# Performance work log

Measured on AMD Instinct MI355X. Metric: run time of the kernel, lower is better.

The kernel has to match this reference:

```python
import jax, jax.numpy as jnp
import numpy as np

KERNELS = [(1, 2), (2, 1), (1, 3), (3, 1), (1, 4), (4, 1), (2, 2)]
IN_C, OUT_C = 16, 64
FC_IN, FC_H1, FC_H2, NUM_ACTIONS = 3648, 512, 128, 4


def setup_inputs() -> dict:
    key = jax.random.key(0)
    ks = jax.random.split(key, 32)
    B = 32768
    inp = {"x": jax.random.normal(ks[0], (B, IN_C, 4, 4), dtype=jnp.float32)}
    # conv params, OIHW layout, scaled like torch default init (~1/sqrt(fan_in))
    for i, (kh, kw) in enumerate(KERNELS):
        fan_in = IN_C * kh * kw
        s = 1.0 / np.sqrt(fan_in)
        inp[f"w{i}"] = jax.random.uniform(ks[1 + 2 * i], (OUT_C, IN_C, kh, kw), jnp.float32, -s, s)
        inp[f"b{i}"] = jax.random.uniform(ks[2 + 2 * i], (OUT_C,), jnp.float32, -s, s)
    dims = [(FC_IN, FC_H1), (FC_H1, FC_H2), (FC_H2, NUM_ACTIONS)]
    for j, (din, dout) in enumerate(dims):
        s = 1.0 / np.sqrt(din)
        inp[f"fw{j}"] = jax.random.uniform(ks[15 + 2 * j], (dout, din), jnp.float32, -s, s)
        inp[f"fb{j}"] = jax.random.uniform(ks[16 + 2 * j], (dout,), jnp.float32, -s, s)
    return inp


def _conv_relu_flat(x, w, b):
    # x: [B,16,4,4] NCHW, w: [64,16,kh,kw] OIHW -> flatten to [B, 64*oh*ow]
    y = jax.lax.conv_general_dilated(
        x, w, window_strides=(1, 1), padding="VALID",
        dimension_numbers=("NCHW", "OIHW", "NCHW"))
    y = jax.nn.relu(y + b[None, :, None, None])
    return y.reshape(y.shape[0], -1)


def reference(x, w0, b0, w1, b1, w2, b2, w3, b3, w4, b4, w5, b5, w6, b6,
              fw0, fb0, fw1, fb1, fw2, fb2):
    x = x.reshape(-1, 16, 4, 4).astype(jnp.float32)
    ws = [w0, w1, w2, w3, w4, w5, w6]
    bs = [b0, b1, b2, b3, b4, b5, b6]
    combined = jnp.concatenate(
        [_conv_relu_flat(x, w, b) for w, b in zip(ws, bs)], axis=1)  # [B, 3648]
    h = jax.nn.relu(combined @ fw0.T + fb0)
    h = jax.nn.relu(h @ fw1.T + fb1)
    return h @ fw2.T + fb2
```

## Files before the change

kernel.cpp:

```cpp
#include <hip/hip_runtime.h>
#include <hip/hip_bf16.h>
#include <stdint.h>

typedef __attribute__((ext_vector_type(8))) short s8v;
typedef __attribute__((ext_vector_type(4))) float f32x4;

__device__ __forceinline__ unsigned short f2bf(float f) {
  unsigned u = __builtin_bit_cast(unsigned, f);
  u += 0x7fffu + ((u >> 16) & 1u);
  return (unsigned short)(u >> 16);
}

__device__ __forceinline__ void gl16(const void* g, void* l) {
  __builtin_amdgcn_global_load_lds(
      (const __attribute__((address_space(1))) unsigned int*)g,
      (__attribute__((address_space(3))) unsigned int*)l,
      16, 0, 0);
}


__global__ void cast_bf16_k(const float* __restrict__ s, unsigned short* __restrict__ d, int n4) {
  int i = blockIdx.x * blockDim.x + threadIdx.x;
  if (i < n4) {
    float4 v = reinterpret_cast<const float4*>(s)[i];
    ushort4 o;
    o.x = f2bf(v.x); o.y = f2bf(v.y); o.z = f2bf(v.z); o.w = f2bf(v.w);
    reinterpret_cast<ushort4*>(d)[i] = o;
  }
}

__global__ void prep_conv(
    const float* w0, const float* w1, const float* w2, const float* w3,
    const float* w4, const float* w5, const float* w6,
    const float* b0, const float* b1, const float* b2, const float* b3,
    const float* b4, const float* b5, const float* b6,
    unsigned short* __restrict__ Mt, float* __restrict__ cbias)
{
  int n = blockIdx.x * blockDim.x + threadIdx.x;
  if (n >= 3712) return;
  unsigned short* row = Mt + n * 256;
  for (int i = 0; i < 256; ++i) row[i] = 0;
  if (n >= 3648) { cbias[n] = 0.f; return; }
  const int khs[7] = {1,2,1,3,1,4,2};
  const int kws[7] = {2,1,3,1,4,1,2};
  const int cs[8]  = {0,768,1536,2048,2560,2816,3072,3648};
  const float* ws[7] = {w0,w1,w2,w3,w4,w5,w6};
  const float* bs[7] = {b0,b1,b2,b3,b4,b5,b6};
  int k = 6;
  while (n < cs[k]) --k;
  const int kh = khs[k], kw = kws[k];
  const int ow = 5 - kw, np = (5 - kh) * ow;
  const int r = n - cs[k];
  const int och = r / np, p = r % np;
  const int oi = p / ow, oj = p % ow;
  const float* w = ws[k];
  cbias[n] = bs[k][och];
  for (int c = 0; c < 16; ++c)
    for (int dh = 0; dh < kh; ++dh)
      for (int dw = 0; dw < kw; ++dw)
        row[c * 16 + (oi + dh) * 4 + (oj + dw)] =
            f2bf(w[((och * 16 + c) * kh + dh) * kw + dw]);
}

__global__ void prep_fw0(const float* __restrict__ fw0, unsigned short* __restrict__ outp) {
  int idx = blockIdx.x * 256 + threadIdx.x;
  int nrow = idx / 3712;
  int k = idx - nrow * 3712;
  outp[idx] = (k < 3648) ? f2bf(fw0[nrow * 3648 + k]) : (unsigned short)0;
}

__global__ __launch_bounds__(512, 2) void fused_conv_fc1(
    const unsigned short* __restrict__ xb,
    const unsigned short* __restrict__ Mt,
    const float* __restrict__ cbias,
    const unsigned short* __restrict__ fw0b,
    const float* __restrict__ fb0,
    unsigned short* __restrict__ h1)
{
  __shared__ unsigned short xs[128 * 256];
  __shared__ unsigned short ms[128 * 128];
  __shared__ unsigned short ps[128 * 128];
  const int tid = threadIdx.x;
  const int lane = tid & 63;
  const int w = tid >> 6;
  const int wm = w >> 2;
  const int wn = w & 3;
  const int g8 = lane >> 4;
  const int l15 = lane & 15;
  const int m0 = blockIdx.x * 128;

  {
    char* dst = (char*)xs + (w * 8) * 1024 + lane * 16;
#pragma unroll
    for (int i = 0; i < 8; ++i) {
      int c = (w * 8 + i) * 64 + lane;
      int row = c >> 5, col16 = c & 31;
      int cs = col16 ^ (row & 7);
      gl16(xb + (size_t)(m0 + row) * 256 + cs * 8, dst + i * 1024);
    }
  }

  f32x4 acc[4][8] = {};

#pragma unroll 1
  for (int j = 0; j < 29; ++j) {
    f32x4 accp[4][2] = {};
    const int ar = wm * 64 + l15;
    const int br = wn * 32 + l15;
#pragma unroll 1
    for (int h = 0; h < 2; ++h) {
      __syncthreads();
      {
        char* dst = (char*)ms + (w * 4) * 1024 + lane * 16;
#pragma unroll
        for (int i = 0; i < 4; ++i) {
          int c = (w * 4 + i) * 64 + lane;
          int row = c >> 4, col16 = c & 15;
          int cs = col16 ^ (row & 7);
          gl16(Mt + (size_t)(j * 128 + row) * 256 + h * 128 + cs * 8, dst + i * 1024);
        }
      }
      __syncthreads();
#pragma unroll
      for (int kk = 0; kk < 4; ++kk) {
        const int cx = h * 16 + kk * 4 + g8;
        const int cm = kk * 4 + g8;
        s8v xa[4], mb[2];
#pragma unroll
        for (int mi = 0; mi < 4; ++mi) {
          int r = ar + mi * 16;
          xa[mi] = *(const s8v*)((const char*)xs + r * 512 + ((cx ^ (r & 7)) << 4));
        }
#pragma unroll
        for (int ni = 0; ni < 2; ++ni) {
          int r = br + ni * 16;
          mb[ni] = *(const s8v*)((const char*)ms + r * 256 + ((cm ^ (r & 7)) << 4));
        }
#pragma unroll
        for (int mi = 0; mi < 4; ++mi)
#pragma unroll
          for (int ni = 0; ni < 2; ++ni)
            accp[mi][ni] = __builtin_amdgcn_mfma_f32_16x16x32_bf16(
                xa[mi], mb[ni], accp[mi][ni], 0, 0, 0);
      }
    }
#pragma unroll
    for (int ni = 0; ni < 2; ++ni) {
      const int pc = wn * 32 + ni * 16 + l15;
      const float bv = cbias[j * 128 + pc];
#pragma unroll
      for (int mi = 0; mi < 4; ++mi) {
#pragma unroll
        for (int r = 0; r < 4; ++r) {
          const int pr = wm * 64 + mi * 16 + g8 * 4 + r;
          float v = accp[mi][ni][r] + bv;
          v = v > 0.f ? v : 0.f;
          *(unsigned short*)((char*)ps + pr * 256 +
                             (((pc >> 3) ^ (pr & 7)) << 4) + (pc & 7) * 2) = f2bf(v);
        }
      }
    }
    __syncthreads();

    const int kbase = j * 128;
#pragma unroll
    for (int kk = 0; kk < 4; ++kk) {
      const int c16 = kk * 4 + g8;
      s8v pa[4], fwb[8];
#pragma unroll
      for (int mi = 0; mi < 4; ++mi) {
        int r = wm * 64 + mi * 16 + l15;
        pa[mi] = *(const s8v*)((const char*)ps + r * 256 + ((c16 ^ (r & 7)) << 4));
      }
      const int kf = kbase + kk * 32 + g8 * 8;
#pragma unroll
      for (int ni = 0; ni < 8; ++ni) {
        int bn = wn * 128 + ni * 16 + l15;
        fwb[ni] = *(const s8v*)(fw0b + (size_t)bn * 3712 + kf);
      }
#pragma unroll
      for (int mi = 0; mi < 4; ++mi)
#pragma unroll
        for (int ni = 0; ni < 8; ++ni)
          acc[mi][ni] = __builtin_amdgcn_mfma_f32_16x16x32_bf16(
              pa[mi], fwb[ni], acc[mi][ni], 0, 0, 0);
    }
  }

#pragma unroll
  for (int ni = 0; ni < 8; ++ni) {
    const int col = wn * 128 + ni * 16 + l15;
    const float bv = fb0[col];
#pragma unroll
    for (int mi = 0; mi < 4; ++mi) {
      const int row = m0 + wm * 64 + mi * 16 + g8 * 4;
#pragma unroll
      for (int r = 0; r < 4; ++r) {
        float v = acc[mi][ni][r] + bv;
        v = v > 0.f ? v : 0.f;
        h1[(size_t)(row + r) * 512 + col] = f2bf(v);
      }
    }
  }
}

__global__ __launch_bounds__(256) void fc23(
    const unsigned short* __restrict__ h1,
    const unsigned short* __restrict__ fw1b,
    const float* __restrict__ fb1,
    const float* __restrict__ fw2,
    const float* __restrict__ fb2,
    float* __restrict__ out)
{
  __shared__ unsigned short As[64 * 64];
  __shared__ unsigned short Bs[128 * 64];
  __shared__ float h2[64][129];
  const int tid = threadIdx.x;
  const int lane = tid & 63;
  const int wave = tid >> 6;
  const int wm = wave >> 1, wn = wave & 1;
  const int m0 = blockIdx.x * 64;

  f32x4 acc[2][4] = {};

  const unsigned short* Ag = h1 + (size_t)(m0 + (lane >> 3)) * 512 + (lane & 7) * 8;
  const unsigned short* Bg = fw1b + (size_t)(lane >> 3) * 512 + (lane & 7) * 8;
  char* Asb = (char*)As + wave * 2048 + lane * 16;
  char* Bsb = (char*)Bs + wave * 4096 + lane * 16;

  for (int k0 = 0; k0 < 512; k0 += 64) {
#pragma unroll
    for (int i = 0; i < 2; ++i)
      gl16(Ag + (size_t)((wave * 2 + i) * 8) * 512 + k0, Asb + i * 1024);
#pragma unroll
    for (int i = 0; i < 4; ++i)
      gl16(Bg + (size_t)((wave * 4 + i) * 8) * 512 + k0, Bsb + i * 1024);
    __syncthreads();
    const int arow = wm * 32 + (lane & 15);
    const int brow = wn * 64 + (lane & 15);
    const int kc = (lane >> 4) * 8;
    s8v af[2][2], bfv[4][2];
#pragma unroll
    for (int mi = 0; mi < 2; ++mi)
#pragma unroll
      for (int kk = 0; kk < 2; ++kk)
        af[mi][kk] = *(const s8v*)(As + (arow + mi * 16) * 64 + kk * 32 + kc);
#pragma unroll
    for (int ni = 0; ni < 4; ++ni)
#pragma unroll
      for (int kk = 0; kk < 2; ++kk)
        bfv[ni][kk] = *(const s8v*)(Bs + (brow + ni * 16) * 64 + kk * 32 + kc);
#pragma unroll
    for (int kk = 0; kk < 2; ++kk)
#pragma unroll
      for (int mi = 0; mi < 2; ++mi)
#pragma unroll
        for (int ni = 0; ni < 4; ++ni)
          acc[mi][ni] = __builtin_amdgcn_mfma_f32_16x16x32_bf16(
              af[mi][kk], bfv[ni][kk], acc[mi][ni], 0, 0, 0);
    __syncthreads();
  }

#pragma unroll
  for (int ni = 0; ni < 4; ++ni) {
    const int col = wn * 64 + ni * 16 + (lane & 15);
    const float bv = fb1[col];
#pragma unroll
    for (int mi = 0; mi < 2; ++mi) {
      const int rl = wm * 32 + mi * 16 + (lane >> 4) * 4;
#pragma unroll
      for (int r = 0; r < 4; ++r) {
        float v = acc[mi][ni][r] + bv;
        h2[rl + r][col] = v > 0.f ? v : 0.f;
      }
    }
  }
  __syncthreads();

  const int r = tid >> 2, j = tid & 3;
  const float* w = fw2 + j * 128;
  float dot = fb2[j];
#pragma unroll 8
  for (int c = 0; c < 128; ++c) dot += h2[r][c] * w[c];
  out[(size_t)(m0 + r) * 4 + j] = dot;
}


extern "C" void kernel_launch(void* const* d_in, const int* in_sizes, int n_in,
                              void* d_out, int out_size, void* d_ws, size_t ws_size,
                              hipStream_t stream) {
  const float* x = (const float*)d_in[0];
  const float* w[7];
  const float* b[7];
  for (int i = 0; i < 7; ++i) {
    w[i] = (const float*)d_in[1 + 2 * i];
    b[i] = (const float*)d_in[2 + 2 * i];
  }
  const float* fw0 = (const float*)d_in[15];
  const float* fb0 = (const float*)d_in[16];
  const float* fw1 = (const float*)d_in[17];
  const float* fb1 = (const float*)d_in[18];
  const float* fw2 = (const float*)d_in[19];
  const float* fb2 = (const float*)d_in[20];

  char* ws = (char*)d_ws;
  size_t off = 0;
  auto alloc = [&](size_t bytes) {
    void* p = ws + off;
    off += (bytes + 255) & ~(size_t)255;
    return p;
  };
  unsigned short* Mt   = (unsigned short*)alloc((size_t)3712 * 256 * 2);
  float*          cb   = (float*)alloc((size_t)3712 * 4);
  unsigned short* fw0b = (unsigned short*)alloc((size_t)512 * 3712 * 2);
  unsigned short* fw1b = (unsigned short*)alloc((size_t)128 * 512 * 2);
  unsigned short* xb   = (unsigned short*)alloc((size_t)32768 * 256 * 2);
  unsigned short* h1   = (unsigned short*)alloc((size_t)32768 * 512 * 2);
  if (ws_size < off) return;

  cast_bf16_k<<<8192, 256, 0, stream>>>(x, xb, 2097152);
  cast_bf16_k<<<64, 256, 0, stream>>>(fw1, fw1b, 16384);
  prep_conv<<<15, 256, 0, stream>>>(w[0], w[1], w[2], w[3], w[4], w[5], w[6],
                                    b[0], b[1], b[2], b[3], b[4], b[5], b[6], Mt, cb);
  prep_fw0<<<7424, 256, 0, stream>>>(fw0, fw0b);

  fused_conv_fc1<<<256, 512, 0, stream>>>(xb, Mt, cb, fw0b, fb0, h1);
  fc23<<<512, 256, 0, stream>>>(h1, fw1b, fb1, fw2, fb2, (float*)d_out);
}
```

Before: 584.4 us.

## Halve fused conv-FC1 row tile and double-buffer conv matrix staging

```diff
diff --git a/kernel.cpp b/kernel.cpp
--- a/kernel.cpp
+++ b/kernel.cpp
@@ -77,9 +77,10 @@
     const float* __restrict__ fb0,
     unsigned short* __restrict__ h1)
 {
-  __shared__ unsigned short xs[128 * 256];
-  __shared__ unsigned short ms[128 * 128];
-  __shared__ unsigned short ps[128 * 128];
+  __shared__ unsigned short xs[64 * 256];
+  __shared__ unsigned short ms0[128 * 128];
+  __shared__ unsigned short ms1[128 * 128];
+  __shared__ unsigned short ps[64 * 128];
   const int tid = threadIdx.x;
   const int lane = tid & 63;
   const int w = tid >> 6;
@@ -87,72 +88,98 @@
   const int wn = w & 3;
   const int g8 = lane >> 4;
   const int l15 = lane & 15;
-  const int m0 = blockIdx.x * 128;
+  const int m0 = blockIdx.x * 64;
+
+  auto stage_ms = [&](unsigned short* ms, int jj, int h) {
+    char* dst = (char*)ms + (w * 4) * 1024 + lane * 16;
+#pragma unroll
+    for (int i = 0; i < 4; ++i) {
+      int c = (w * 4 + i) * 64 + lane;
+      int row = c >> 4, col16 = c & 15;
+      gl16(Mt + (size_t)(jj * 128 + row) * 256 + h * 128 + (col16 ^ (row & 7)) * 8,
+           dst + i * 1024);
+    }
+  };
 
   {
-    char* dst = (char*)xs + (w * 8) * 1024 + lane * 16;
-#pragma unroll
-    for (int i = 0; i < 8; ++i) {
-      int c = (w * 8 + i) * 64 + lane;
+    char* dst = (char*)xs + (w * 4) * 1024 + lane * 16;
+#pragma unroll
+    for (int i = 0; i < 4; ++i) {
+      int c = (w * 4 + i) * 64 + lane;
       int row = c >> 5, col16 = c & 31;
-      int cs = col16 ^ (row & 7);
-      gl16(xb + (size_t)(m0 + row) * 256 + cs * 8, dst + i * 1024);
-    }
-  }
-
-  f32x4 acc[4][8] = {};
+      gl16(xb + (size_t)(m0 + row) * 256 + (col16 ^ (row & 7)) * 8, dst + i * 1024);
+    }
+  }
+  stage_ms(ms0, 0, 0);
+  stage_ms(ms1, 0, 1);
+  __syncthreads();
+
+  f32x4 acc[2][8] = {};
+  const int ar = wm * 32 + l15;
 
 #pragma unroll 1
   for (int j = 0; j < 29; ++j) {
-    f32x4 accp[4][2] = {};
-    const int ar = wm * 64 + l15;
-    const int br = wn * 32 + l15;
-#pragma unroll 1
-    for (int h = 0; h < 2; ++h) {
-      __syncthreads();
-      {
-        char* dst = (char*)ms + (w * 4) * 1024 + lane * 16;
-#pragma unroll
-        for (int i = 0; i < 4; ++i) {
-          int c = (w * 4 + i) * 64 + lane;
-          int row = c >> 4, col16 = c & 15;
-          int cs = col16 ^ (row & 7);
-          gl16(Mt + (size_t)(j * 128 + row) * 256 + h * 128 + cs * 8, dst + i * 1024);
-        }
-      }
-      __syncthreads();
-#pragma unroll
-      for (int kk = 0; kk < 4; ++kk) {
-        const int cx = h * 16 + kk * 4 + g8;
-        const int cm = kk * 4 + g8;
-        s8v xa[4], mb[2];
-#pragma unroll
-        for (int mi = 0; mi < 4; ++mi) {
-          int r = ar + mi * 16;
-          xa[mi] = *(const s8v*)((const char*)xs + r * 512 + ((cx ^ (r & 7)) << 4));
-        }
-#pragma unroll
-        for (int ni = 0; ni < 2; ++ni) {
-          int r = br + ni * 16;
-          mb[ni] = *(const s8v*)((const char*)ms + r * 256 + ((cm ^ (r & 7)) << 4));
-        }
-#pragma unroll
-        for (int mi = 0; mi < 4; ++mi)
-#pragma unroll
-          for (int ni = 0; ni < 2; ++ni)
-            accp[mi][ni] = __builtin_amdgcn_mfma_f32_16x16x32_bf16(
-                xa[mi], mb[ni], accp[mi][ni], 0, 0, 0);
-      }
-    }
+    const int jn = (j < 28) ? j + 1 : 0;
+    f32x4 accp[2][2] = {};
+
+#pragma unroll
+    for (int kk = 0; kk < 4; ++kk) {
+      const int cx = kk * 4 + g8;
+      s8v xa[2], mb[2];
+#pragma unroll
+      for (int mi = 0; mi < 2; ++mi) {
+        int r = ar + mi * 16;
+        xa[mi] = *(const s8v*)((const char*)xs + r * 512 + ((cx ^ (r & 7)) << 4));
+      }
+#pragma unroll
+      for (int ni = 0; ni < 2; ++ni) {
+        int r = wn * 32 + ni * 16 + l15;
+        mb[ni] = *(const s8v*)((const char*)ms0 + r * 256 + ((cx ^ (r & 7)) << 4));
+      }
+#pragma unroll
+      for (int mi = 0; mi < 2; ++mi)
+#pragma unroll
+        for (int ni = 0; ni < 2; ++ni)
+          accp[mi][ni] = __builtin_amdgcn_mfma_f32_16x16x32_bf16(
+              xa[mi], mb[ni], accp[mi][ni], 0, 0, 0);
+    }
+    __syncthreads();
+
+    stage_ms(ms0, jn, 0);
+
+#pragma unroll
+    for (int kk = 0; kk < 4; ++kk) {
+      const int cm = kk * 4 + g8;
+      const int cx = 16 + cm;
+      s8v xa[2], mb[2];
+#pragma unroll
+      for (int mi = 0; mi < 2; ++mi) {
+        int r = ar + mi * 16;
+        xa[mi] = *(const s8v*)((const char*)xs + r * 512 + ((cx ^ (r & 7)) << 4));
+      }
+#pragma unroll
+      for (int ni = 0; ni < 2; ++ni) {
+        int r = wn * 32 + ni * 16 + l15;
+        mb[ni] = *(const s8v*)((const char*)ms1 + r * 256 + ((cm ^ (r & 7)) << 4));
+      }
+#pragma unroll
+      for (int mi = 0; mi < 2; ++mi)
+#pragma unroll
+        for (int ni = 0; ni < 2; ++ni)
+          accp[mi][ni] = __builtin_amdgcn_mfma_f32_16x16x32_bf16(
+              xa[mi], mb[ni], accp[mi][ni], 0, 0, 0);
+    }
+    __syncthreads();
+
 #pragma unroll
     for (int ni = 0; ni < 2; ++ni) {
       const int pc = wn * 32 + ni * 16 + l15;
       const float bv = cbias[j * 128 + pc];
 #pragma unroll
-      for (int mi = 0; mi < 4; ++mi) {
+      for (int mi = 0; mi < 2; ++mi) {
 #pragma unroll
         for (int r = 0; r < 4; ++r) {
-          const int pr = wm * 64 + mi * 16 + g8 * 4 + r;
+          const int pr = wm * 32 + mi * 16 + g8 * 4 + r;
           float v = accp[mi][ni][r] + bv;
           v = v > 0.f ? v : 0.f;
           *(unsigned short*)((char*)ps + pr * 256 +
@@ -162,24 +189,25 @@
     }
     __syncthreads();
 
-    const int kbase = j * 128;
+    stage_ms(ms1, jn, 1);
+
 #pragma unroll
     for (int kk = 0; kk < 4; ++kk) {
       const int c16 = kk * 4 + g8;
-      s8v pa[4], fwb[8];
-#pragma unroll
-      for (int mi = 0; mi < 4; ++mi) {
-        int r = wm * 64 + mi * 16 + l15;
+      s8v pa[2], fwb[8];
+#pragma unroll
+      for (int mi = 0; mi < 2; ++mi) {
+        int r = wm * 32 + mi * 16 + l15;
         pa[mi] = *(const s8v*)((const char*)ps + r * 256 + ((c16 ^ (r & 7)) << 4));
       }
-      const int kf = kbase + kk * 32 + g8 * 8;
+      const int kf = j * 128 + kk * 32 + g8 * 8;
 #pragma unroll
       for (int ni = 0; ni < 8; ++ni) {
         int bn = wn * 128 + ni * 16 + l15;
         fwb[ni] = *(const s8v*)(fw0b + (size_t)bn * 3712 + kf);
       }
 #pragma unroll
-      for (int mi = 0; mi < 4; ++mi)
+      for (int mi = 0; mi < 2; ++mi)
 #pragma unroll
         for (int ni = 0; ni < 8; ++ni)
           acc[mi][ni] = __builtin_amdgcn_mfma_f32_16x16x32_bf16(
@@ -192,8 +220,8 @@
     const int col = wn * 128 + ni * 16 + l15;
     const float bv = fb0[col];
 #pragma unroll
-    for (int mi = 0; mi < 4; ++mi) {
-      const int row = m0 + wm * 64 + mi * 16 + g8 * 4;
+    for (int mi = 0; mi < 2; ++mi) {
+      const int row = m0 + wm * 32 + mi * 16 + g8 * 4;
 #pragma unroll
       for (int r = 0; r < 4; ++r) {
         float v = acc[mi][ni][r] + bv;
@@ -324,6 +352,6 @@
                                     b[0], b[1], b[2], b[3], b[4], b[5], b[6], Mt, cb);
   prep_fw0<<<7424, 256, 0, stream>>>(fw0, fw0b);
 
-  fused_conv_fc1<<<256, 512, 0, stream>>>(xb, Mt, cb, fw0b, fb0, h1);
+  fused_conv_fc1<<<512, 512, 0, stream>>>(xb, Mt, cb, fw0b, fb0, h1);
   fc23<<<512, 256, 0, stream>>>(h1, fw1b, fb1, fw2, fb2, (float*)d_out);
 }
```

New measurement: 704.5 us. +20.6%, slower.

## Prepack weights into MFMA fragment order and pipeline conv with FC1 tiles

Applied to the files above, without the earlier changes.

```diff
diff --git a/kernel.cpp b/kernel.cpp
--- a/kernel.cpp
+++ b/kernel.cpp
@@ -29,130 +29,124 @@
   }
 }
 
-__global__ void prep_conv(
+__global__ void prep_convF(
     const float* w0, const float* w1, const float* w2, const float* w3,
     const float* w4, const float* w5, const float* w6,
     const float* b0, const float* b1, const float* b2, const float* b3,
     const float* b4, const float* b5, const float* b6,
-    unsigned short* __restrict__ Mt, float* __restrict__ cbias)
+    unsigned short* __restrict__ MtF, float* __restrict__ cbias)
 {
   int n = blockIdx.x * blockDim.x + threadIdx.x;
   if (n >= 3712) return;
-  unsigned short* row = Mt + n * 256;
-  for (int i = 0; i < 256; ++i) row[i] = 0;
+  const int j = n >> 7, nn = n & 127, tile = nn >> 4, ln = nn & 15;
+  auto put = [&](int k, unsigned short v) {
+    int kk = k >> 5, gk = (k >> 3) & 3, e = k & 7;
+    MtF[(size_t)((((j * 8 + kk) * 8 + tile) * 64 + ln * 4 + gk) * 8 + e)] = v;
+  };
+  for (int k = 0; k < 256; ++k) put(k, 0);
   if (n >= 3648) { cbias[n] = 0.f; return; }
   const int khs[7] = {1,2,1,3,1,4,2};
   const int kws[7] = {2,1,3,1,4,1,2};
   const int cs[8]  = {0,768,1536,2048,2560,2816,3072,3648};
   const float* ws[7] = {w0,w1,w2,w3,w4,w5,w6};
   const float* bs[7] = {b0,b1,b2,b3,b4,b5,b6};
-  int k = 6;
-  while (n < cs[k]) --k;
-  const int kh = khs[k], kw = kws[k];
+  int kern = 6;
+  while (n < cs[kern]) --kern;
+  const int kh = khs[kern], kw = kws[kern];
   const int ow = 5 - kw, np = (5 - kh) * ow;
-  const int r = n - cs[k];
+  const int r = n - cs[kern];
   const int och = r / np, p = r % np;
   const int oi = p / ow, oj = p % ow;
-  const float* w = ws[k];
-  cbias[n] = bs[k][och];
+  const float* w = ws[kern];
+  cbias[n] = bs[kern][och];
   for (int c = 0; c < 16; ++c)
     for (int dh = 0; dh < kh; ++dh)
       for (int dw = 0; dw < kw; ++dw)
-        row[c * 16 + (oi + dh) * 4 + (oj + dw)] =
-            f2bf(w[((och * 16 + c) * kh + dh) * kw + dw]);
-}
-
-__global__ void prep_fw0(const float* __restrict__ fw0, unsigned short* __restrict__ outp) {
+        put(c * 16 + (oi + dh) * 4 + (oj + dw),
+            f2bf(w[((och * 16 + c) * kh + dh) * kw + dw]));
+}
+
+__global__ void prep_fw0F(const float* __restrict__ fw0, unsigned short* __restrict__ outp) {
   int idx = blockIdx.x * 256 + threadIdx.x;
   int nrow = idx / 3712;
   int k = idx - nrow * 3712;
-  outp[idx] = (k < 3648) ? f2bf(fw0[nrow * 3648 + k]) : (unsigned short)0;
-}
-
-__global__ __launch_bounds__(512, 2) void fused_conv_fc1(
+  const int j = k >> 7, kk = (k >> 5) & 3, gk = (k >> 3) & 3, e = k & 7;
+  const int tile = nrow >> 4, ln = nrow & 15;
+  outp[(size_t)((((j * 4 + kk) * 32 + tile) * 64 + ln * 4 + gk) * 8 + e)] =
+      (k < 3648) ? f2bf(fw0[nrow * 3648 + k]) : (unsigned short)0;
+}
+
+__global__ __launch_bounds__(512, 4) void fused_conv_fc1(
     const unsigned short* __restrict__ xb,
-    const unsigned short* __restrict__ Mt,
+    const unsigned short* __restrict__ MtF,
     const float* __restrict__ cbias,
-    const unsigned short* __restrict__ fw0b,
+    const unsigned short* __restrict__ fwF,
     const float* __restrict__ fb0,
     unsigned short* __restrict__ h1)
 {
-  __shared__ unsigned short xs[128 * 256];
-  __shared__ unsigned short ms[128 * 128];
-  __shared__ unsigned short ps[128 * 128];
+  __shared__ unsigned short xs[64 * 256];
+  __shared__ unsigned short ps[64 * 128];
   const int tid = threadIdx.x;
   const int lane = tid & 63;
   const int w = tid >> 6;
-  const int wm = w >> 2;
-  const int wn = w & 3;
   const int g8 = lane >> 4;
   const int l15 = lane & 15;
-  const int m0 = blockIdx.x * 128;
+  const int m0 = blockIdx.x * 64;
+  const int cwm = w >> 2;
+  const int cwn = w & 3;
 
   {
-    char* dst = (char*)xs + (w * 8) * 1024 + lane * 16;
-#pragma unroll
-    for (int i = 0; i < 8; ++i) {
-      int c = (w * 8 + i) * 64 + lane;
+    char* dst = (char*)xs + w * 4096 + lane * 16;
+#pragma unroll
+    for (int i = 0; i < 4; ++i) {
+      int c = (w * 4 + i) * 64 + lane;
       int row = c >> 5, col16 = c & 31;
-      int cs = col16 ^ (row & 7);
-      gl16(xb + (size_t)(m0 + row) * 256 + cs * 8, dst + i * 1024);
-    }
-  }
-
-  f32x4 acc[4][8] = {};
-
-#pragma unroll 1
-  for (int j = 0; j < 29; ++j) {
-    f32x4 accp[4][2] = {};
-    const int ar = wm * 64 + l15;
-    const int br = wn * 32 + l15;
-#pragma unroll 1
-    for (int h = 0; h < 2; ++h) {
-      __syncthreads();
-      {
-        char* dst = (char*)ms + (w * 4) * 1024 + lane * 16;
-#pragma unroll
-        for (int i = 0; i < 4; ++i) {
-          int c = (w * 4 + i) * 64 + lane;
-          int row = c >> 4, col16 = c & 15;
-          int cs = col16 ^ (row & 7);
-          gl16(Mt + (size_t)(j * 128 + row) * 256 + h * 128 + cs * 8, dst + i * 1024);
-        }
-      }
-      __syncthreads();
-#pragma unroll
-      for (int kk = 0; kk < 4; ++kk) {
-        const int cx = h * 16 + kk * 4 + g8;
-        const int cm = kk * 4 + g8;
-        s8v xa[4], mb[2];
-#pragma unroll
-        for (int mi = 0; mi < 4; ++mi) {
-          int r = ar + mi * 16;
-          xa[mi] = *(const s8v*)((const char*)xs + r * 512 + ((cx ^ (r & 7)) << 4));
-        }
-#pragma unroll
-        for (int ni = 0; ni < 2; ++ni) {
-          int r = br + ni * 16;
-          mb[ni] = *(const s8v*)((const char*)ms + r * 256 + ((cm ^ (r & 7)) << 4));
-        }
-#pragma unroll
-        for (int mi = 0; mi < 4; ++mi)
-#pragma unroll
-          for (int ni = 0; ni < 2; ++ni)
-            accp[mi][ni] = __builtin_amdgcn_mfma_f32_16x16x32_bf16(
-                xa[mi], mb[ni], accp[mi][ni], 0, 0, 0);
-      }
-    }
+      gl16(xb + (size_t)(m0 + row) * 256 + (col16 ^ (row & 7)) * 8, dst + i * 1024);
+    }
+  }
+  __syncthreads();
+
+  f32x4 acc[4][4] = {};
+  f32x4 accp[2][2];
+
+  auto conv = [&](int jj) {
+#pragma unroll
+    for (int mi = 0; mi < 2; ++mi)
+#pragma unroll
+      for (int ni = 0; ni < 2; ++ni)
+        accp[mi][ni] = f32x4{0.f, 0.f, 0.f, 0.f};
+    const unsigned short* mtj = MtF + (size_t)jj * 32768;
+#pragma unroll
+    for (int kk = 0; kk < 8; ++kk) {
+      s8v xa[2], mb[2];
+#pragma unroll
+      for (int mi = 0; mi < 2; ++mi) {
+        int r = cwm * 32 + mi * 16 + l15;
+        xa[mi] = *(const s8v*)((const char*)xs + r * 512 +
+                               (((kk * 4 + g8) ^ (r & 7)) << 4));
+      }
+#pragma unroll
+      for (int ni = 0; ni < 2; ++ni)
+        mb[ni] = *(const s8v*)(mtj + ((kk * 8 + cwn * 2 + ni) * 64 + l15 * 4 + g8) * 8);
+#pragma unroll
+      for (int mi = 0; mi < 2; ++mi)
+#pragma unroll
+        for (int ni = 0; ni < 2; ++ni)
+          accp[mi][ni] = __builtin_amdgcn_mfma_f32_16x16x32_bf16(
+              xa[mi], mb[ni], accp[mi][ni], 0, 0, 0);
+    }
+  };
+
+  auto pwrite = [&](int jj) {
 #pragma unroll
     for (int ni = 0; ni < 2; ++ni) {
-      const int pc = wn * 32 + ni * 16 + l15;
-      const float bv = cbias[j * 128 + pc];
-#pragma unroll
-      for (int mi = 0; mi < 4; ++mi) {
+      const int pc = cwn * 32 + ni * 16 + l15;
+      const float bv = cbias[jj * 128 + pc];
+#pragma unroll
+      for (int mi = 0; mi < 2; ++mi) {
 #pragma unroll
         for (int r = 0; r < 4; ++r) {
-          const int pr = wm * 64 + mi * 16 + g8 * 4 + r;
+          const int pr = cwm * 32 + mi * 16 + g8 * 4 + r;
           float v = accp[mi][ni][r] + bv;
           v = v > 0.f ? v : 0.f;
           *(unsigned short*)((char*)ps + pr * 256 +
@@ -160,40 +154,47 @@
         }
       }
     }
-    __syncthreads();
-
-    const int kbase = j * 128;
+  };
+
+  conv(0);
+  pwrite(0);
+  __syncthreads();
+
+#pragma unroll 1
+  for (int j = 0; j < 29; ++j) {
+    if (j < 28) conv(j + 1);
+    const unsigned short* fwj = fwF + (size_t)j * 65536;
 #pragma unroll
     for (int kk = 0; kk < 4; ++kk) {
-      const int c16 = kk * 4 + g8;
-      s8v pa[4], fwb[8];
+      s8v pa[4], fwb[4];
 #pragma unroll
       for (int mi = 0; mi < 4; ++mi) {
-        int r = wm * 64 + mi * 16 + l15;
-        pa[mi] = *(const s8v*)((const char*)ps + r * 256 + ((c16 ^ (r & 7)) << 4));
-      }
-      const int kf = kbase + kk * 32 + g8 * 8;
-#pragma unroll
-      for (int ni = 0; ni < 8; ++ni) {
-        int bn = wn * 128 + ni * 16 + l15;
-        fwb[ni] = *(const s8v*)(fw0b + (size_t)bn * 3712 + kf);
-      }
+        int r = mi * 16 + l15;
+        pa[mi] = *(const s8v*)((const char*)ps + r * 256 +
+                               (((kk * 4 + g8) ^ (r & 7)) << 4));
+      }
+#pragma unroll
+      for (int ni = 0; ni < 4; ++ni)
+        fwb[ni] = *(const s8v*)(fwj + ((kk * 32 + w * 4 + ni) * 64 + l15 * 4 + g8) * 8);
 #pragma unroll
       for (int mi = 0; mi < 4; ++mi)
 #pragma unroll
-        for (int ni = 0; ni < 8; ++ni)
+        for (int ni = 0; ni < 4; ++ni)
           acc[mi][ni] = __builtin_amdgcn_mfma_f32_16x16x32_bf16(
               pa[mi], fwb[ni], acc[mi][ni], 0, 0, 0);
     }
-  }
-
-#pragma unroll
-  for (int ni = 0; ni < 8; ++ni) {
-    const int col = wn * 128 + ni * 16 + l15;
+    __syncthreads();
+    if (j < 28) pwrite(j + 1);
+    __syncthreads();
+  }
+
+#pragma unroll
+  for (int ni = 0; ni < 4; ++ni) {
+    const int col = w * 64 + ni * 16 + l15;
     const float bv = fb0[col];
 #pragma unroll
     for (int mi = 0; mi < 4; ++mi) {
-      const int row = m0 + wm * 64 + mi * 16 + g8 * 4;
+      const int row = m0 + mi * 16 + g8 * 4;
 #pragma unroll
       for (int r = 0; r < 4; ++r) {
         float v = acc[mi][ni][r] + bv;
@@ -310,9 +311,9 @@
     off += (bytes + 255) & ~(size_t)255;
     return p;
   };
-  unsigned short* Mt   = (unsigned short*)alloc((size_t)3712 * 256 * 2);
+  unsigned short* MtF  = (unsigned short*)alloc((size_t)3712 * 256 * 2);
   float*          cb   = (float*)alloc((size_t)3712 * 4);
-  unsigned short* fw0b = (unsigned short*)alloc((size_t)512 * 3712 * 2);
+  unsigned short* fwF  = (unsigned short*)alloc((size_t)512 * 3712 * 2);
   unsigned short* fw1b = (unsigned short*)alloc((size_t)128 * 512 * 2);
   unsigned short* xb   = (unsigned short*)alloc((size_t)32768 * 256 * 2);
   unsigned short* h1   = (unsigned short*)alloc((size_t)32768 * 512 * 2);
@@ -320,10 +321,10 @@
 
   cast_bf16_k<<<8192, 256, 0, stream>>>(x, xb, 2097152);
   cast_bf16_k<<<64, 256, 0, stream>>>(fw1, fw1b, 16384);
-  prep_conv<<<15, 256, 0, stream>>>(w[0], w[1], w[2], w[3], w[4], w[5], w[6],
-                                    b[0], b[1], b[2], b[3], b[4], b[5], b[6], Mt, cb);
-  prep_fw0<<<7424, 256, 0, stream>>>(fw0, fw0b);
-
-  fused_conv_fc1<<<256, 512, 0, stream>>>(xb, Mt, cb, fw0b, fb0, h1);
+  prep_convF<<<15, 256, 0, stream>>>(w[0], w[1], w[2], w[3], w[4], w[5], w[6],
+                                     b[0], b[1], b[2], b[3], b[4], b[5], b[6], MtF, cb);
+  prep_fw0F<<<7424, 256, 0, stream>>>(fw0, fwF);
+
+  fused_conv_fc1<<<512, 512, 0, stream>>>(xb, MtF, cb, fwF, fb0, h1);
   fc23<<<512, 256, 0, stream>>>(h1, fw1b, fb1, fw2, fb2, (float*)d_out);
 }
```

Result: slower. 714.1 us (+22.2%).
